# Kernel optimization log

Hardware: AMD Instinct MI355X
Metric: run time of the kernel (lower is better)

The kernel has to match this reference:

```python
import jax, jax.numpy as jnp
import numpy as np

EPS = 1e-12  # F.normalize eps


def setup_inputs() -> dict:
    key = jax.random.key(0)
    k1, k2 = jax.random.split(key)
    bs, d = 8192, 128
    data = jax.random.normal(k1, (bs, d), dtype=jnp.float32)
    label = jax.random.randint(k2, (bs, 1), 0, 2, dtype=jnp.int64)
    scale = jnp.asarray(np.log(1.0 / 0.07), dtype=jnp.float32)  # learned temperature param
    return {"data": data, "scale": scale, "label": label}


def reference(data, scale, label):
    bs = data.shape[0]
    # L2-normalize rows (F.normalize semantics with eps clamp)
    norm = jnp.maximum(jnp.linalg.norm(data, axis=-1, keepdims=True), EPS)
    x = data / norm
    logits = (x @ x.T) * jnp.exp(scale)  # [bs, bs]
    # Vectorized equivalent of the python double loop: binary same-class matrix
    sim = (label == label.T).astype(logits.dtype)  # [bs, bs]
    q = jax.nn.softmax(sim / jnp.sum(sim, axis=-1, keepdims=True), axis=-1)
    p = jax.nn.log_softmax(logits, axis=-1)
    log_q = jnp.log(q)  # q > 0 always (softmax output)
    # F.kl_div(p, q, 'batchmean') = sum(q * (log q - p)) / bs
    loss1 = jnp.sum(q * (log_q - p)) / bs
    # F.kl_div(q.log(), p.exp(), 'batchmean') = sum(exp(p) * (p - log q)) / bs
    loss2 = jnp.sum(jnp.exp(p) * (p - log_q)) / bs
    return (loss1 + loss2) * 0.5
```

## Files before the change

kernel.cpp:

```cpp
#include <hip/hip_runtime.h>
#include <stdint.h>

#define BS 8192
#define DD 128
#define L2E 1.4426950408889634f
#define LN2 0.6931471805599453f

typedef __attribute__((ext_vector_type(8))) short short8;
typedef __attribute__((ext_vector_type(4))) float float4v;

#if __has_builtin(__builtin_amdgcn_exp2f)
#define EXP2(x) __builtin_amdgcn_exp2f(x)
#else
#define EXP2(x) exp2f(x)
#endif

__device__ __forceinline__ float bf2f(short s) {
  union { unsigned u; float f; } c;
  c.u = ((unsigned)(unsigned short)s) << 16;
  return c.f;
}
__device__ __forceinline__ short f2bf(float f) {
  union { float f; unsigned u; } c; c.f = f;
  unsigned u = c.u + 0x7FFFu + ((c.u >> 16) & 1u);
  return (short)(u >> 16);
}


__global__ __launch_bounds__(256) void k_norm(const float* __restrict__ data,
                                              const int* __restrict__ label,
                                              char* __restrict__ xnbF,
                                              float* __restrict__ gh8,
                                              int* __restrict__ cnt8,
                                              float* __restrict__ Zr,
                                              float* __restrict__ Ur,
                                              float* __restrict__ Vr,
                                              float* __restrict__ mf) {
  __shared__ float shg[256];
  __shared__ int shc[2];
  int tid = threadIdx.x, wave = tid >> 6, lane = tid & 63;
  int lh = lane & 31, rsel = lane >> 5;
  if (tid < 2) shc[tid] = 0;
  shg[tid] = 0.f;
  int rowbase = blockIdx.x * 32;
  if (tid < 32) {
    int row = rowbase + tid;
    Zr[row] = 0.f; Ur[row] = 0.f; Vr[row] = 0.f;
    mf[row] = (label[row] == 0) ? 1.f : 0.f;
  }
  __syncthreads();

  float a00 = 0.f, a01 = 0.f, a02 = 0.f, a03 = 0.f;
  float a10 = 0.f, a11 = 0.f, a12 = 0.f, a13 = 0.f;
  int c0 = 0, c1 = 0;
#pragma unroll
  for (int it = 0; it < 4; ++it) {
    int row = rowbase + it * 8 + wave * 2 + rsel;
    float4 v = *(const float4*)&data[row * DD + lh * 4];
    float ss = v.x * v.x + v.y * v.y + v.z * v.z + v.w * v.w;
#pragma unroll
    for (int off = 16; off; off >>= 1) ss += __shfl_xor(ss, off);
    float rn = 1.f / fmaxf(sqrtf(ss), 1e-12f);
    float x0 = v.x * rn, x1 = v.y * rn, x2 = v.z * rn, x3 = v.w * rn;

    unsigned pk0 = (unsigned)(unsigned short)f2bf(x0) |
                   ((unsigned)(unsigned short)f2bf(x1) << 16);
    unsigned pk1 = (unsigned)(unsigned short)f2bf(x2) |
                   ((unsigned)(unsigned short)f2bf(x3) << 16);
    int kc = lh >> 1;
    size_t chunk = (size_t)(row >> 4) * 256 + (size_t)(kc >> 2) * 64 +
                   (size_t)(kc & 3) * 16 + (row & 15);
    *(uint2*)(xnbF + chunk * 16 + (lh & 1) * 8) = make_uint2(pk0, pk1);

    int lab = label[row];
    if (lab == 0) {
      a00 += x0; a01 += x1; a02 += x2; a03 += x3;
      if (lh == 0) c0++;
    } else {
      a10 += x0; a11 += x1; a12 += x2; a13 += x3;
      if (lh == 0) c1++;
    }
  }
  int base = lh * 4;
  atomicAdd(&shg[base + 0], a00); atomicAdd(&shg[base + 1], a01);
  atomicAdd(&shg[base + 2], a02); atomicAdd(&shg[base + 3], a03);
  atomicAdd(&shg[128 + base + 0], a10); atomicAdd(&shg[128 + base + 1], a11);
  atomicAdd(&shg[128 + base + 2], a12); atomicAdd(&shg[128 + base + 3], a13);
  if (lh == 0) { atomicAdd(&shc[0], c0); atomicAdd(&shc[1], c1); }
  __syncthreads();
  atomicAdd(&gh8[(blockIdx.x & 7) * 256 + tid], shg[tid]);
  if (tid < 2) atomicAdd(&cnt8[(blockIdx.x & 7) * 2 + tid], shc[tid]);
}

__global__ __launch_bounds__(512, 4) void k_main(const short* __restrict__ xnbF,
                                                 const int* __restrict__ label,
                                                 const float* __restrict__ mf,
                                                 const float* __restrict__ scale,
                                                 float* __restrict__ Zr,
                                                 float* __restrict__ Ur,
                                                 float* __restrict__ Vr) {
  __shared__ short tile[2][64 * DD];
  int tid = threadIdx.x, wave = tid >> 6, lane = tid & 63;
  int quad = lane >> 4, col = lane & 15;
  int rbI = blockIdx.x >> 4;
  int sl = blockIdx.x & 15;
  float se2 = __expf(scale[0]) * L2E;

  const short8* F = (const short8*)xnbF;

  int gA = rbI * 16 + wave * 2;
  short8 af[2][4];
#pragma unroll
  for (int s = 0; s < 2; ++s)
#pragma unroll
    for (int t = 0; t < 4; ++t) {
      short8 a = F[(size_t)(gA + s) * 256 + t * 64 + lane];
#pragma unroll
      for (int i = 0; i < 8; ++i) a[i] = f2bf(bf2f(a[i]) * se2);
      af[s][t] = a;
    }

  float4v Z0 = {0.f,0.f,0.f,0.f}, Z1 = Z0, U0 = Z0, U1 = Z0, V0 = Z0, V1 = Z0;

  int cb4 = sl * 32;

#define STAGE(buf, jt)                                                         \
  {                                                                            \
    const char* s_ = (const char*)xnbF +                                       \
                     ((size_t)(cb4 + (jt) * 4) * 256 + tid) * 16;              \
    char* d_ = (char*)tile[buf] + tid * 16;                                    \
    __builtin_amdgcn_global_load_lds(                                          \
        (const __attribute__((address_space(1))) void*)(uintptr_t)s_,          \
        (__attribute__((address_space(3))) void*)(uintptr_t)d_, 16, 0, 0);     \
    __builtin_amdgcn_global_load_lds(                                          \
        (const __attribute__((address_space(1))) void*)(uintptr_t)(s_ + 8192), \
        (__attribute__((address_space(3))) void*)(uintptr_t)(d_ + 8192),       \
        16, 0, 0);                                                             \
  }

  STAGE(0, 0);
  __syncthreads();

#pragma unroll 1
  for (int jt = 0; jt < 8; ++jt) {
    if (jt < 7) STAGE((jt + 1) & 1, jt + 1);
    const short8* T8 = (const short8*)tile[jt & 1];
    int jcb = sl * 512 + jt * 64;

#define HALFTILE(jo)                                                           \
    {                                                                          \
      short8 b00 = T8[(jo) * 256 + lane];                                      \
      short8 b01 = T8[(jo) * 256 + 64 + lane];                                 \
      short8 b02 = T8[(jo) * 256 + 128 + lane];                                \
      short8 b03 = T8[(jo) * 256 + 192 + lane];                                \
      short8 b10 = T8[(jo + 1) * 256 + lane];                                  \
      short8 b11 = T8[(jo + 1) * 256 + 64 + lane];                             \
      short8 b12 = T8[(jo + 1) * 256 + 128 + lane];                            \
      short8 b13 = T8[(jo + 1) * 256 + 192 + lane];                            \
      float m0 = mf[jcb + (jo) * 16 + col];                                    \
      float m1 = mf[jcb + (jo + 1) * 16 + col];                                \
      float4v c00 = {0.f, 0.f, 0.f, 0.f}, c01 = c00, c10 = c00, c11 = c00;     \
      c00 = __builtin_amdgcn_mfma_f32_16x16x32_bf16(af[0][0], b00, c00, 0,0,0);\
      c01 = __builtin_amdgcn_mfma_f32_16x16x32_bf16(af[1][0], b00, c01, 0,0,0);\
      c10 = __builtin_amdgcn_mfma_f32_16x16x32_bf16(af[0][0], b10, c10, 0,0,0);\
      c11 = __builtin_amdgcn_mfma_f32_16x16x32_bf16(af[1][0], b10, c11, 0,0,0);\
      c00 = __builtin_amdgcn_mfma_f32_16x16x32_bf16(af[0][1], b01, c00, 0,0,0);\
      c01 = __builtin_amdgcn_mfma_f32_16x16x32_bf16(af[1][1], b01, c01, 0,0,0);\
      c10 = __builtin_amdgcn_mfma_f32_16x16x32_bf16(af[0][1], b11, c10, 0,0,0);\
      c11 = __builtin_amdgcn_mfma_f32_16x16x32_bf16(af[1][1], b11, c11, 0,0,0);\
      c00 = __builtin_amdgcn_mfma_f32_16x16x32_bf16(af[0][2], b02, c00, 0,0,0);\
      c01 = __builtin_amdgcn_mfma_f32_16x16x32_bf16(af[1][2], b02, c01, 0,0,0);\
      c10 = __builtin_amdgcn_mfma_f32_16x16x32_bf16(af[0][2], b12, c10, 0,0,0);\
      c11 = __builtin_amdgcn_mfma_f32_16x16x32_bf16(af[1][2], b12, c11, 0,0,0);\
      c00 = __builtin_amdgcn_mfma_f32_16x16x32_bf16(af[0][3], b03, c00, 0,0,0);\
      c01 = __builtin_amdgcn_mfma_f32_16x16x32_bf16(af[1][3], b03, c01, 0,0,0);\
      c10 = __builtin_amdgcn_mfma_f32_16x16x32_bf16(af[0][3], b13, c10, 0,0,0);\
      c11 = __builtin_amdgcn_mfma_f32_16x16x32_bf16(af[1][3], b13, c11, 0,0,0);\
      _Pragma("unroll")                                                        \
      for (int r = 0; r < 4; ++r) {  \
        float l, e;                                                            \
        l = c00[r]; e = EXP2(l);        \
        Z0[r] += e; U0[r] = fmaf(e, l, U0[r]); V0[r] = fmaf(m0, e, V0[r]);     \
        l = c01[r]; e = EXP2(l);                                               \
        Z1[r] += e; U1[r] = fmaf(e, l, U1[r]); V1[r] = fmaf(m0, e, V1[r]);     \
        l = c10[r]; e = EXP2(l);                                               \
        Z0[r] += e; U0[r] = fmaf(e, l, U0[r]); V0[r] = fmaf(m1, e, V0[r]);     \
        l = c11[r]; e = EXP2(l);                                               \
        Z1[r] += e; U1[r] = fmaf(e, l, U1[r]); V1[r] = fmaf(m1, e, V1[r]);     \
      }                                                                        \
    }
    HALFTILE(0)
    HALFTILE(2)
#undef HALFTILE
    __syncthreads();
  }
#undef STAGE

#define EMIT(s, Zc, Uc, Vc)                                                    \
  {                                                                            \
    _Pragma("unroll")                                                          \
    for (int r = 0; r < 4; ++r) {                                              \
      float z = Zc[r], u = Uc[r], v0 = Vc[r];                                  \
      _Pragma("unroll")                                                        \
      for (int off = 1; off < 16; off <<= 1) {                                 \
        z += __shfl_xor(z, off);                                               \
        u += __shfl_xor(u, off);                                               \
        v0 += __shfl_xor(v0, off);                                             \
      }                                                                        \
      if (col == 0) {                                                          \
        int row = rbI * 256 + wave * 32 + s * 16 + quad * 4 + r;               \
        int lab = label[row];                                                  \
        float v = (lab == 0) ? v0 : (z - v0);                                  \
        atomicAdd(&Zr[row], z);                                                \
        atomicAdd(&Ur[row], u * LN2);                 \
        atomicAdd(&Vr[row], v);                                                \
      }                                                                        \
    }                                                                          \
  }
  EMIT(0, Z0, U0, V0)
  EMIT(1, Z1, U1, V1)
#undef EMIT
}

__global__ __launch_bounds__(256) void k_final(const float* __restrict__ data,
                                               const int* __restrict__ label,
                                               const float* __restrict__ scale,
                                               const float* __restrict__ gh8,
                                               const int* __restrict__ cnt8,
                                               const float* __restrict__ Zr,
                                               const float* __restrict__ Ur,
                                               const float* __restrict__ Vr,
                                               float* __restrict__ partial,
                                               int* __restrict__ ticket,
                                               float* __restrict__ out) {
  __shared__ float hsum[256];
  __shared__ float bsum[4];
  __shared__ int lastb;
  int tid = threadIdx.x, wave = tid >> 6, lane = tid & 63;
  int lh = lane & 31, rsel = lane >> 5;
  float hs = 0.f;
#pragma unroll
  for (int i = 0; i < 8; ++i) hs += gh8[i * 256 + tid];
  hsum[tid] = hs;
  __syncthreads();

  float se = __expf(scale[0]);
  int ci0 = 0, ci1 = 0;
#pragma unroll
  for (int i = 0; i < 8; ++i) { ci0 += cnt8[2 * i]; ci1 += cnt8[2 * i + 1]; }
  float c0 = (float)ci0, c1 = (float)ci1;
  float4 h0 = *(const float4*)&hsum[lh * 4];
  float4 h1 = *(const float4*)&hsum[128 + lh * 4];

  float local = 0.f;
#pragma unroll
  for (int it = 0; it < 4; ++it) {
    int row = blockIdx.x * 32 + it * 8 + wave * 2 + rsel;
    float4 v = *(const float4*)&data[row * DD + lh * 4];
    float ss = v.x * v.x + v.y * v.y + v.z * v.z + v.w * v.w;
#pragma unroll
    for (int off = 16; off; off >>= 1) ss += __shfl_xor(ss, off);
    float rn = 1.f / fmaxf(sqrtf(ss), 1e-12f);

    int lab = label[row];
    float sg = v.x * (h0.x + h1.x) + v.y * (h0.y + h1.y) +
               v.z * (h0.z + h1.z) + v.w * (h0.w + h1.w);
    float sh_ = (lab == 0)
                    ? (v.x * h0.x + v.y * h0.y + v.z * h0.z + v.w * h0.w)
                    : (v.x * h1.x + v.y * h1.y + v.z * h1.z + v.w * h1.w);
#pragma unroll
    for (int off = 16; off; off >>= 1) {
      sg += __shfl_xor(sg, off);
      sh_ += __shfl_xor(sh_, off);
    }
    if (lh == 0) {
      float cc = (lab == 0) ? c0 : c1;
      float a = __expf(1.f / cc);
      float Zq = cc * a + ((float)BS - cc);
      float S = se * sg * rn, T = se * sh_ * rn;
      float Zv = Zr[row], Uv = Ur[row], Vv = Vr[row];
      local += a / Zq - (S + (a - 1.f) * T) / Zq + Uv / Zv - Vv / (cc * Zv);
    }
  }
#pragma unroll
  for (int off = 32; off; off >>= 1) local += __shfl_xor(local, off);
  if (lane == 0) bsum[wave] = local;
  __syncthreads();
  if (tid == 0) {
    float psum = bsum[0] + bsum[1] + bsum[2] + bsum[3];
    __hip_atomic_store(&partial[blockIdx.x], psum, __ATOMIC_RELEASE,
                       __HIP_MEMORY_SCOPE_AGENT);
    int t = __hip_atomic_fetch_add(ticket, 1, __ATOMIC_ACQ_REL,
                                   __HIP_MEMORY_SCOPE_AGENT);
    lastb = (t == 255);
  }
  __syncthreads();
  if (lastb) {
    float v = __hip_atomic_load(&partial[tid], __ATOMIC_ACQUIRE,
                                __HIP_MEMORY_SCOPE_AGENT);
#pragma unroll
    for (int off = 32; off; off >>= 1) v += __shfl_xor(v, off);
    if (lane == 0) bsum[wave] = v;
    __syncthreads();
    if (tid == 0)
      out[0] = (bsum[0] + bsum[1] + bsum[2] + bsum[3]) * (0.5f / (float)BS);
  }
}

extern "C" void kernel_launch(void* const* d_in, const int* in_sizes, int n_in,
                              void* d_out, int out_size, void* d_ws, size_t ws_size,
                              hipStream_t stream) {
  const float* data = (const float*)d_in[0];
  const float* scale = (const float*)d_in[1];
  const int* label = (const int*)d_in[2];
  char* ws = (char*)d_ws;
  char* xnbF = ws;
  float* Zr = (float*)(ws + 2097152);
  float* Ur = (float*)(ws + 2129920);
  float* Vr = (float*)(ws + 2162688);
  float* gh8 = (float*)(ws + 2195456);
  int* cnt8 = (int*)(ws + 2203648);
  int* ticket = (int*)(ws + 2203712);
  float* partial = (float*)(ws + 2203716);
  float* mf = (float*)(ws + 2204800);

  hipMemsetAsync(ws + 2195456, 0, 8260, stream);

  k_norm<<<256, 256, 0, stream>>>(data, label, xnbF, gh8, cnt8, Zr, Ur, Vr, mf);
  k_main<<<512, 512, 0, stream>>>((const short*)xnbF, label, mf, scale, Zr, Ur, Vr);
  k_final<<<256, 256, 0, stream>>>(data, label, scale, gh8, cnt8, Zr, Ur, Vr,
                                   partial, ticket, (float*)d_out);
}
```

Baseline: 108.7 us.

## Exploit Gram matrix symmetry by computing only upper-triangle block pairs

The main kernel now iterates over upper-triangular block pairs (bi<=bj) of the symmetric logits matrix. Off-diagonal tiles feed both row sums and, through per-column reductions and atomics, column sums, which roughly halves the MFMA and exp work. In exchange it adds cross-lane shuffles and many global atomics per tile, and uses a serial loop to decode the triangular index. The norm and final kernels get twice as many smaller blocks and 16-way partial accumulators to match.

After: 162.3 us. +49.3%, slower.

```diff
diff --git a/kernel.cpp b/kernel.cpp
--- a/kernel.cpp
+++ b/kernel.cpp
@@ -30,8 +30,8 @@
 __global__ __launch_bounds__(256) void k_norm(const float* __restrict__ data,
                                               const int* __restrict__ label,
                                               char* __restrict__ xnbF,
-                                              float* __restrict__ gh8,
-                                              int* __restrict__ cnt8,
+                                              float* __restrict__ gh16,
+                                              int* __restrict__ cnt16,
                                               float* __restrict__ Zr,
                                               float* __restrict__ Ur,
                                               float* __restrict__ Vr,
@@ -42,8 +42,8 @@
   int lh = lane & 31, rsel = lane >> 5;
   if (tid < 2) shc[tid] = 0;
   shg[tid] = 0.f;
-  int rowbase = blockIdx.x * 32;
-  if (tid < 32) {
+  int rowbase = blockIdx.x * 16;
+  if (tid < 16) {
     int row = rowbase + tid;
     Zr[row] = 0.f; Ur[row] = 0.f; Vr[row] = 0.f;
     mf[row] = (label[row] == 0) ? 1.f : 0.f;
@@ -54,7 +54,7 @@
   float a10 = 0.f, a11 = 0.f, a12 = 0.f, a13 = 0.f;
   int c0 = 0, c1 = 0;
 #pragma unroll
-  for (int it = 0; it < 4; ++it) {
+  for (int it = 0; it < 2; ++it) {
     int row = rowbase + it * 8 + wave * 2 + rsel;
     float4 v = *(const float4*)&data[row * DD + lh * 4];
     float ss = v.x * v.x + v.y * v.y + v.z * v.z + v.w * v.w;
@@ -88,8 +88,8 @@
   atomicAdd(&shg[128 + base + 2], a12); atomicAdd(&shg[128 + base + 3], a13);
   if (lh == 0) { atomicAdd(&shc[0], c0); atomicAdd(&shc[1], c1); }
   __syncthreads();
-  atomicAdd(&gh8[(blockIdx.x & 7) * 256 + tid], shg[tid]);
-  if (tid < 2) atomicAdd(&cnt8[(blockIdx.x & 7) * 2 + tid], shc[tid]);
+  atomicAdd(&gh16[(blockIdx.x & 15) * 256 + tid], shg[tid]);
+  if (tid < 2) atomicAdd(&cnt16[(blockIdx.x & 15) * 2 + tid], shc[tid]);
 }
 
 __global__ __launch_bounds__(512, 4) void k_main(const short* __restrict__ xnbF,
@@ -102,32 +102,45 @@
   __shared__ short tile[2][64 * DD];
   int tid = threadIdx.x, wave = tid >> 6, lane = tid & 63;
   int quad = lane >> 4, col = lane & 15;
-  int rbI = blockIdx.x >> 4;
-  int sl = blockIdx.x & 15;
+  int job = blockIdx.x;
+  int t = job >> 1, half = job & 1;
+  int bi = 0, rem = t;
+  while (rem >= 32 - bi) { rem -= 32 - bi; ++bi; }
+  int bj = bi + rem;
+  bool offd = (bi != bj);
   float se2 = __expf(scale[0]) * L2E;
 
   const short8* F = (const short8*)xnbF;
 
-  int gA = rbI * 16 + wave * 2;
+  int gA = bi * 16 + wave * 2;
   short8 af[2][4];
 #pragma unroll
   for (int s = 0; s < 2; ++s)
 #pragma unroll
-    for (int t = 0; t < 4; ++t) {
-      short8 a = F[(size_t)(gA + s) * 256 + t * 64 + lane];
+    for (int tt = 0; tt < 4; ++tt) {
+      short8 a = F[(size_t)(gA + s) * 256 + tt * 64 + lane];
 #pragma unroll
       for (int i = 0; i < 8; ++i) a[i] = f2bf(bf2f(a[i]) * se2);
-      af[s][t] = a;
-    }
+      af[s][tt] = a;
+    }
+
+  int rowb = bi * 256 + wave * 32;
+  float mr0[4], mr1[4];
+#pragma unroll
+  for (int r = 0; r < 4; ++r) {
+    mr0[r] = mf[rowb + quad * 4 + r];
+    mr1[r] = mf[rowb + 16 + quad * 4 + r];
+  }
 
   float4v Z0 = {0.f,0.f,0.f,0.f}, Z1 = Z0, U0 = Z0, U1 = Z0, V0 = Z0, V1 = Z0;
 
-  int cb4 = sl * 32;
-
-#define STAGE(buf, jt)                                                         \
+  int cgb = bj * 16 + half * 8;
+  int jbase = bj * 256 + half * 128;
+
+#define STAGE(buf, st)                                                         \
   {                                                                            \
     const char* s_ = (const char*)xnbF +                                       \
-                     ((size_t)(cb4 + (jt) * 4) * 256 + tid) * 16;              \
+                     ((size_t)(cgb + (st) * 4) * 256 + tid) * 16;              \
     char* d_ = (char*)tile[buf] + tid * 16;                                    \
     __builtin_amdgcn_global_load_lds(                                          \
         (const __attribute__((address_space(1))) void*)(uintptr_t)s_,          \
@@ -142,56 +155,50 @@
   __syncthreads();
 
 #pragma unroll 1
-  for (int jt = 0; jt < 8; ++jt) {
-    if (jt < 7) STAGE((jt + 1) & 1, jt + 1);
-    const short8* T8 = (const short8*)tile[jt & 1];
-    int jcb = sl * 512 + jt * 64;
-
-#define HALFTILE(jo)                                                           \
-    {                                                                          \
-      short8 b00 = T8[(jo) * 256 + lane];                                      \
-      short8 b01 = T8[(jo) * 256 + 64 + lane];                                 \
-      short8 b02 = T8[(jo) * 256 + 128 + lane];                                \
-      short8 b03 = T8[(jo) * 256 + 192 + lane];                                \
-      short8 b10 = T8[(jo + 1) * 256 + lane];                                  \
-      short8 b11 = T8[(jo + 1) * 256 + 64 + lane];                             \
-      short8 b12 = T8[(jo + 1) * 256 + 128 + lane];                            \
-      short8 b13 = T8[(jo + 1) * 256 + 192 + lane];                            \
-      float m0 = mf[jcb + (jo) * 16 + col];                                    \
-      float m1 = mf[jcb + (jo + 1) * 16 + col];                                \
-      float4v c00 = {0.f, 0.f, 0.f, 0.f}, c01 = c00, c10 = c00, c11 = c00;     \
-      c00 = __builtin_amdgcn_mfma_f32_16x16x32_bf16(af[0][0], b00, c00, 0,0,0);\
-      c01 = __builtin_amdgcn_mfma_f32_16x16x32_bf16(af[1][0], b00, c01, 0,0,0);\
-      c10 = __builtin_amdgcn_mfma_f32_16x16x32_bf16(af[0][0], b10, c10, 0,0,0);\
-      c11 = __builtin_amdgcn_mfma_f32_16x16x32_bf16(af[1][0], b10, c11, 0,0,0);\
-      c00 = __builtin_amdgcn_mfma_f32_16x16x32_bf16(af[0][1], b01, c00, 0,0,0);\
-      c01 = __builtin_amdgcn_mfma_f32_16x16x32_bf16(af[1][1], b01, c01, 0,0,0);\
-      c10 = __builtin_amdgcn_mfma_f32_16x16x32_bf16(af[0][1], b11, c10, 0,0,0);\
-      c11 = __builtin_amdgcn_mfma_f32_16x16x32_bf16(af[1][1], b11, c11, 0,0,0);\
-      c00 = __builtin_amdgcn_mfma_f32_16x16x32_bf16(af[0][2], b02, c00, 0,0,0);\
-      c01 = __builtin_amdgcn_mfma_f32_16x16x32_bf16(af[1][2], b02, c01, 0,0,0);\
-      c10 = __builtin_amdgcn_mfma_f32_16x16x32_bf16(af[0][2], b12, c10, 0,0,0);\
-      c11 = __builtin_amdgcn_mfma_f32_16x16x32_bf16(af[1][2], b12, c11, 0,0,0);\
-      c00 = __builtin_amdgcn_mfma_f32_16x16x32_bf16(af[0][3], b03, c00, 0,0,0);\
-      c01 = __builtin_amdgcn_mfma_f32_16x16x32_bf16(af[1][3], b03, c01, 0,0,0);\
-      c10 = __builtin_amdgcn_mfma_f32_16x16x32_bf16(af[0][3], b13, c10, 0,0,0);\
-      c11 = __builtin_amdgcn_mfma_f32_16x16x32_bf16(af[1][3], b13, c11, 0,0,0);\
-      _Pragma("unroll")                                                        \
-      for (int r = 0; r < 4; ++r) {  \
-        float l, e;                                                            \
-        l = c00[r]; e = EXP2(l);        \
-        Z0[r] += e; U0[r] = fmaf(e, l, U0[r]); V0[r] = fmaf(m0, e, V0[r]);     \
-        l = c01[r]; e = EXP2(l);                                               \
-        Z1[r] += e; U1[r] = fmaf(e, l, U1[r]); V1[r] = fmaf(m0, e, V1[r]);     \
-        l = c10[r]; e = EXP2(l);                                               \
-        Z0[r] += e; U0[r] = fmaf(e, l, U0[r]); V0[r] = fmaf(m1, e, V0[r]);     \
-        l = c11[r]; e = EXP2(l);                                               \
-        Z1[r] += e; U1[r] = fmaf(e, l, U1[r]); V1[r] = fmaf(m1, e, V1[r]);     \
-      }                                                                        \
-    }
-    HALFTILE(0)
-    HALFTILE(2)
-#undef HALFTILE
+  for (int st = 0; st < 2; ++st) {
+    if (st == 0) STAGE(1, 1);
+    const short8* T8 = (const short8*)tile[st];
+    int jcb = jbase + st * 64;
+#pragma unroll
+    for (int jo = 0; jo < 4; ++jo) {
+      short8 b0 = T8[jo * 256 + lane];
+      short8 b1 = T8[jo * 256 + 64 + lane];
+      short8 b2 = T8[jo * 256 + 128 + lane];
+      short8 b3 = T8[jo * 256 + 192 + lane];
+      float m0 = mf[jcb + jo * 16 + col];
+      float4v c0 = {0.f, 0.f, 0.f, 0.f}, c1 = c0;
+      c0 = __builtin_amdgcn_mfma_f32_16x16x32_bf16(af[0][0], b0, c0, 0, 0, 0);
+      c1 = __builtin_amdgcn_mfma_f32_16x16x32_bf16(af[1][0], b0, c1, 0, 0, 0);
+      c0 = __builtin_amdgcn_mfma_f32_16x16x32_bf16(af[0][1], b1, c0, 0, 0, 0);
+      c1 = __builtin_amdgcn_mfma_f32_16x16x32_bf16(af[1][1], b1, c1, 0, 0, 0);
+      c0 = __builtin_amdgcn_mfma_f32_16x16x32_bf16(af[0][2], b2, c0, 0, 0, 0);
+      c1 = __builtin_amdgcn_mfma_f32_16x16x32_bf16(af[1][2], b2, c1, 0, 0, 0);
+      c0 = __builtin_amdgcn_mfma_f32_16x16x32_bf16(af[0][3], b3, c0, 0, 0, 0);
+      c1 = __builtin_amdgcn_mfma_f32_16x16x32_bf16(af[1][3], b3, c1, 0, 0, 0);
+      float zc = 0.f, uc = 0.f, vc = 0.f;
+#pragma unroll
+      for (int r = 0; r < 4; ++r) {
+        float l = c0[r], e = EXP2(l);
+        Z0[r] += e; U0[r] = fmaf(e, l, U0[r]); V0[r] = fmaf(m0, e, V0[r]);
+        zc += e; uc = fmaf(e, l, uc); vc = fmaf(mr0[r], e, vc);
+        l = c1[r]; e = EXP2(l);
+        Z1[r] += e; U1[r] = fmaf(e, l, U1[r]); V1[r] = fmaf(m0, e, V1[r]);
+        zc += e; uc = fmaf(e, l, uc); vc = fmaf(mr1[r], e, vc);
+      }
+      if (offd) {
+        zc += __shfl_xor(zc, 16); uc += __shfl_xor(uc, 16);
+        vc += __shfl_xor(vc, 16);
+        zc += __shfl_xor(zc, 32); uc += __shfl_xor(uc, 32);
+        vc += __shfl_xor(vc, 32);
+        if (quad == 0) {
+          int jc = jcb + jo * 16 + col;
+          atomicAdd(&Zr[jc], zc);
+          atomicAdd(&Ur[jc], uc * LN2);
+          float vcol = (m0 != 0.f) ? vc : (zc - vc);
+          atomicAdd(&Vr[jc], vcol);
+        }
+      }
+    }
     __syncthreads();
   }
 #undef STAGE
@@ -208,7 +215,7 @@
         v0 += __shfl_xor(v0, off);                                             \
       }                                                                        \
       if (col == 0) {                                                          \
-        int row = rbI * 256 + wave * 32 + s * 16 + quad * 4 + r;               \
+        int row = rowb + s * 16 + quad * 4 + r;                                \
         int lab = label[row];                                                  \
         float v = (lab == 0) ? v0 : (z - v0);                                  \
         atomicAdd(&Zr[row], z);                                                \
@@ -225,8 +232,8 @@
 __global__ __launch_bounds__(256) void k_final(const float* __restrict__ data,
                                                const int* __restrict__ label,
                                                const float* __restrict__ scale,
-                                               const float* __restrict__ gh8,
-                                               const int* __restrict__ cnt8,
+                                               const float* __restrict__ gh16,
+                                               const int* __restrict__ cnt16,
                                                const float* __restrict__ Zr,
                                                const float* __restrict__ Ur,
                                                const float* __restrict__ Vr,
@@ -240,22 +247,22 @@
   int lh = lane & 31, rsel = lane >> 5;
   float hs = 0.f;
 #pragma unroll
-  for (int i = 0; i < 8; ++i) hs += gh8[i * 256 + tid];
+  for (int i = 0; i < 16; ++i) hs += gh16[i * 256 + tid];
   hsum[tid] = hs;
   __syncthreads();
 
   float se = __expf(scale[0]);
   int ci0 = 0, ci1 = 0;
 #pragma unroll
-  for (int i = 0; i < 8; ++i) { ci0 += cnt8[2 * i]; ci1 += cnt8[2 * i + 1]; }
+  for (int i = 0; i < 16; ++i) { ci0 += cnt16[2 * i]; ci1 += cnt16[2 * i + 1]; }
   float c0 = (float)ci0, c1 = (float)ci1;
   float4 h0 = *(const float4*)&hsum[lh * 4];
   float4 h1 = *(const float4*)&hsum[128 + lh * 4];
 
   float local = 0.f;
 #pragma unroll
-  for (int it = 0; it < 4; ++it) {
-    int row = blockIdx.x * 32 + it * 8 + wave * 2 + rsel;
+  for (int it = 0; it < 2; ++it) {
+    int row = blockIdx.x * 16 + it * 8 + wave * 2 + rsel;
     float4 v = *(const float4*)&data[row * DD + lh * 4];
     float ss = v.x * v.x + v.y * v.y + v.z * v.z + v.w * v.w;
 #pragma unroll
@@ -292,11 +299,13 @@
                        __HIP_MEMORY_SCOPE_AGENT);
     int t = __hip_atomic_fetch_add(ticket, 1, __ATOMIC_ACQ_REL,
                                    __HIP_MEMORY_SCOPE_AGENT);
-    lastb = (t == 255);
+    lastb = (t == 511);
   }
   __syncthreads();
   if (lastb) {
     float v = __hip_atomic_load(&partial[tid], __ATOMIC_ACQUIRE,
+                                __HIP_MEMORY_SCOPE_AGENT) +
+              __hip_atomic_load(&partial[tid + 256], __ATOMIC_ACQUIRE,
                                 __HIP_MEMORY_SCOPE_AGENT);
 #pragma unroll
     for (int off = 32; off; off >>= 1) v += __shfl_xor(v, off);
@@ -318,16 +327,16 @@
   float* Zr = (float*)(ws + 2097152);
   float* Ur = (float*)(ws + 2129920);
   float* Vr = (float*)(ws + 2162688);
-  float* gh8 = (float*)(ws + 2195456);
-  int* cnt8 = (int*)(ws + 2203648);
-  int* ticket = (int*)(ws + 2203712);
-  float* partial = (float*)(ws + 2203716);
-  float* mf = (float*)(ws + 2204800);
-
-  hipMemsetAsync(ws + 2195456, 0, 8260, stream);
-
-  k_norm<<<256, 256, 0, stream>>>(data, label, xnbF, gh8, cnt8, Zr, Ur, Vr, mf);
-  k_main<<<512, 512, 0, stream>>>((const short*)xnbF, label, mf, scale, Zr, Ur, Vr);
-  k_final<<<256, 256, 0, stream>>>(data, label, scale, gh8, cnt8, Zr, Ur, Vr,
+  float* gh16 = (float*)(ws + 2195456);
+  int* cnt16 = (int*)(ws + 2211840);
+  int* ticket = (int*)(ws + 2211968);
+  float* partial = (float*)(ws + 2211972);
+  float* mf = (float*)(ws + 2214020);
+
+  hipMemsetAsync(ws + 2195456, 0, 16516, stream);
+
+  k_norm<<<512, 256, 0, stream>>>(data, label, xnbF, gh16, cnt16, Zr, Ur, Vr, mf);
+  k_main<<<1056, 512, 0, stream>>>((const short*)xnbF, label, mf, scale, Zr, Ur, Vr);
+  k_final<<<512, 256, 0, stream>>>(data, label, scale, gh16, cnt16, Zr, Ur, Vr,
                                    partial, ticket, (float*)d_out);
 }
```

## Fold final reduction into main kernel and accumulate logit sums in-loop

Applied to the files above, without the earlier changes.

Removes the k_final kernel and the per-class feature-sum histogram in k_norm. The main GEMM loop now also accumulates the raw logit sum and the same-class logit sum per row, which replaces the separate data re-read and dot-product pass. The last-arriving block of k_main, detected with a ticket counter, computes the final loss. This saves one kernel launch and the extra pass over the data, at the cost of extra ALU work and two more atomics per row inside the hot loop, plus a serial tail reduction on a single block. k_norm is also relaunched with more, smaller blocks.

Measured after the change: 117.1 us. 7.7% more time.

```diff
diff --git a/kernel.cpp b/kernel.cpp
--- a/kernel.cpp
+++ b/kernel.cpp
@@ -30,31 +30,22 @@
 __global__ __launch_bounds__(256) void k_norm(const float* __restrict__ data,
                                               const int* __restrict__ label,
                                               char* __restrict__ xnbF,
-                                              float* __restrict__ gh8,
-                                              int* __restrict__ cnt8,
                                               float* __restrict__ Zr,
                                               float* __restrict__ Ur,
                                               float* __restrict__ Vr,
+                                              float* __restrict__ Wr,
+                                              float* __restrict__ Xr,
                                               float* __restrict__ mf) {
-  __shared__ float shg[256];
-  __shared__ int shc[2];
   int tid = threadIdx.x, wave = tid >> 6, lane = tid & 63;
   int lh = lane & 31, rsel = lane >> 5;
-  if (tid < 2) shc[tid] = 0;
-  shg[tid] = 0.f;
-  int rowbase = blockIdx.x * 32;
-  if (tid < 32) {
+  int rowbase = blockIdx.x * 16;
+  if (tid < 16) {
     int row = rowbase + tid;
-    Zr[row] = 0.f; Ur[row] = 0.f; Vr[row] = 0.f;
+    Zr[row] = 0.f; Ur[row] = 0.f; Vr[row] = 0.f; Wr[row] = 0.f; Xr[row] = 0.f;
     mf[row] = (label[row] == 0) ? 1.f : 0.f;
   }
-  __syncthreads();
-
-  float a00 = 0.f, a01 = 0.f, a02 = 0.f, a03 = 0.f;
-  float a10 = 0.f, a11 = 0.f, a12 = 0.f, a13 = 0.f;
-  int c0 = 0, c1 = 0;
-#pragma unroll
-  for (int it = 0; it < 4; ++it) {
+#pragma unroll
+  for (int it = 0; it < 2; ++it) {
     int row = rowbase + it * 8 + wave * 2 + rsel;
     float4 v = *(const float4*)&data[row * DD + lh * 4];
     float ss = v.x * v.x + v.y * v.y + v.z * v.z + v.w * v.w;
@@ -71,25 +62,7 @@
     size_t chunk = (size_t)(row >> 4) * 256 + (size_t)(kc >> 2) * 64 +
                    (size_t)(kc & 3) * 16 + (row & 15);
     *(uint2*)(xnbF + chunk * 16 + (lh & 1) * 8) = make_uint2(pk0, pk1);
-
-    int lab = label[row];
-    if (lab == 0) {
-      a00 += x0; a01 += x1; a02 += x2; a03 += x3;
-      if (lh == 0) c0++;
-    } else {
-      a10 += x0; a11 += x1; a12 += x2; a13 += x3;
-      if (lh == 0) c1++;
-    }
-  }
-  int base = lh * 4;
-  atomicAdd(&shg[base + 0], a00); atomicAdd(&shg[base + 1], a01);
-  atomicAdd(&shg[base + 2], a02); atomicAdd(&shg[base + 3], a03);
-  atomicAdd(&shg[128 + base + 0], a10); atomicAdd(&shg[128 + base + 1], a11);
-  atomicAdd(&shg[128 + base + 2], a12); atomicAdd(&shg[128 + base + 3], a13);
-  if (lh == 0) { atomicAdd(&shc[0], c0); atomicAdd(&shc[1], c1); }
-  __syncthreads();
-  atomicAdd(&gh8[(blockIdx.x & 7) * 256 + tid], shg[tid]);
-  if (tid < 2) atomicAdd(&cnt8[(blockIdx.x & 7) * 2 + tid], shc[tid]);
+  }
 }
 
 __global__ __launch_bounds__(512, 4) void k_main(const short* __restrict__ xnbF,
@@ -98,8 +71,15 @@
                                                  const float* __restrict__ scale,
                                                  float* __restrict__ Zr,
                                                  float* __restrict__ Ur,
-                                                 float* __restrict__ Vr) {
+                                                 float* __restrict__ Vr,
+                                                 float* __restrict__ Wr,
+                                                 float* __restrict__ Xr,
+                                                 int* __restrict__ ticket,
+                                                 float* __restrict__ out) {
   __shared__ short tile[2][64 * DD];
+  __shared__ int credu[8];
+  __shared__ float fredu[8];
+  __shared__ int lastf;
   int tid = threadIdx.x, wave = tid >> 6, lane = tid & 63;
   int quad = lane >> 4, col = lane & 15;
   int rbI = blockIdx.x >> 4;
@@ -107,7 +87,6 @@
   float se2 = __expf(scale[0]) * L2E;
 
   const short8* F = (const short8*)xnbF;
-
   int gA = rbI * 16 + wave * 2;
   short8 af[2][4];
 #pragma unroll
@@ -121,7 +100,7 @@
     }
 
   float4v Z0 = {0.f,0.f,0.f,0.f}, Z1 = Z0, U0 = Z0, U1 = Z0, V0 = Z0, V1 = Z0;
-
+  float4v W0 = Z0, W1 = Z0, X0 = Z0, X1 = Z0;
   int cb4 = sl * 32;
 
 #define STAGE(buf, jt)                                                         \
@@ -181,12 +160,16 @@
         float l, e;                                                            \
         l = c00[r]; e = EXP2(l);        \
         Z0[r] += e; U0[r] = fmaf(e, l, U0[r]); V0[r] = fmaf(m0, e, V0[r]);     \
+        W0[r] += l; X0[r] = fmaf(m0, l, X0[r]);                                \
         l = c01[r]; e = EXP2(l);                                               \
         Z1[r] += e; U1[r] = fmaf(e, l, U1[r]); V1[r] = fmaf(m0, e, V1[r]);     \
+        W1[r] += l; X1[r] = fmaf(m0, l, X1[r]);                                \
         l = c10[r]; e = EXP2(l);                                               \
         Z0[r] += e; U0[r] = fmaf(e, l, U0[r]); V0[r] = fmaf(m1, e, V0[r]);     \
+        W0[r] += l; X0[r] = fmaf(m1, l, X0[r]);                                \
         l = c11[r]; e = EXP2(l);                                               \
         Z1[r] += e; U1[r] = fmaf(e, l, U1[r]); V1[r] = fmaf(m1, e, V1[r]);     \
+        W1[r] += l; X1[r] = fmaf(m1, l, X1[r]);                                \
       }                                                                        \
     }
     HALFTILE(0)
@@ -196,114 +179,89 @@
   }
 #undef STAGE
 
-#define EMIT(s, Zc, Uc, Vc)                                                    \
+#define EMIT(s, Zc, Uc, Vc, Wc, Xc)                                            \
   {                                                                            \
     _Pragma("unroll")                                                          \
     for (int r = 0; r < 4; ++r) {                                              \
-      float z = Zc[r], u = Uc[r], v0 = Vc[r];                                  \
+      float z = Zc[r], u = Uc[r], v0 = Vc[r], w = Wc[r], x0 = Xc[r];           \
       _Pragma("unroll")                                                        \
       for (int off = 1; off < 16; off <<= 1) {                                 \
         z += __shfl_xor(z, off);                                               \
         u += __shfl_xor(u, off);                                               \
         v0 += __shfl_xor(v0, off);                                             \
+        w += __shfl_xor(w, off);                                               \
+        x0 += __shfl_xor(x0, off);                                             \
       }                                                                        \
       if (col == 0) {                                                          \
         int row = rbI * 256 + wave * 32 + s * 16 + quad * 4 + r;               \
         int lab = label[row];                                                  \
         float v = (lab == 0) ? v0 : (z - v0);                                  \
+        float x = (lab == 0) ? x0 : (w - x0);                                  \
         atomicAdd(&Zr[row], z);                                                \
         atomicAdd(&Ur[row], u * LN2);                 \
         atomicAdd(&Vr[row], v);                                                \
+        atomicAdd(&Wr[row], w * LN2);        \
+        atomicAdd(&Xr[row], x * LN2);                         \
       }                                                                        \
     }                                                                          \
   }
-  EMIT(0, Z0, U0, V0)
-  EMIT(1, Z1, U1, V1)
+  EMIT(0, Z0, U0, V0, W0, X0)
+  EMIT(1, Z1, U1, V1, W1, X1)
 #undef EMIT
-}
-
-__global__ __launch_bounds__(256) void k_final(const float* __restrict__ data,
-                                               const int* __restrict__ label,
-                                               const float* __restrict__ scale,
-                                               const float* __restrict__ gh8,
-                                               const int* __restrict__ cnt8,
-                                               const float* __restrict__ Zr,
-                                               const float* __restrict__ Ur,
-                                               const float* __restrict__ Vr,
-                                               float* __restrict__ partial,
-                                               int* __restrict__ ticket,
-                                               float* __restrict__ out) {
-  __shared__ float hsum[256];
-  __shared__ float bsum[4];
-  __shared__ int lastb;
-  int tid = threadIdx.x, wave = tid >> 6, lane = tid & 63;
-  int lh = lane & 31, rsel = lane >> 5;
-  float hs = 0.f;
-#pragma unroll
-  for (int i = 0; i < 8; ++i) hs += gh8[i * 256 + tid];
-  hsum[tid] = hs;
-  __syncthreads();
-
-  float se = __expf(scale[0]);
-  int ci0 = 0, ci1 = 0;
-#pragma unroll
-  for (int i = 0; i < 8; ++i) { ci0 += cnt8[2 * i]; ci1 += cnt8[2 * i + 1]; }
-  float c0 = (float)ci0, c1 = (float)ci1;
-  float4 h0 = *(const float4*)&hsum[lh * 4];
-  float4 h1 = *(const float4*)&hsum[128 + lh * 4];
-
-  float local = 0.f;
-#pragma unroll
-  for (int it = 0; it < 4; ++it) {
-    int row = blockIdx.x * 32 + it * 8 + wave * 2 + rsel;
-    float4 v = *(const float4*)&data[row * DD + lh * 4];
-    float ss = v.x * v.x + v.y * v.y + v.z * v.z + v.w * v.w;
-#pragma unroll
-    for (int off = 16; off; off >>= 1) ss += __shfl_xor(ss, off);
-    float rn = 1.f / fmaxf(sqrtf(ss), 1e-12f);
-
-    int lab = label[row];
-    float sg = v.x * (h0.x + h1.x) + v.y * (h0.y + h1.y) +
-               v.z * (h0.z + h1.z) + v.w * (h0.w + h1.w);
-    float sh_ = (lab == 0)
-                    ? (v.x * h0.x + v.y * h0.y + v.z * h0.z + v.w * h0.w)
-                    : (v.x * h1.x + v.y * h1.y + v.z * h1.z + v.w * h1.w);
-#pragma unroll
-    for (int off = 16; off; off >>= 1) {
-      sg += __shfl_xor(sg, off);
-      sh_ += __shfl_xor(sh_, off);
-    }
-    if (lh == 0) {
-      float cc = (lab == 0) ? c0 : c1;
-      float a = __expf(1.f / cc);
-      float Zq = cc * a + ((float)BS - cc);
-      float S = se * sg * rn, T = se * sh_ * rn;
-      float Zv = Zr[row], Uv = Ur[row], Vv = Vr[row];
-      local += a / Zq - (S + (a - 1.f) * T) / Zq + Uv / Zv - Vv / (cc * Zv);
-    }
-  }
-#pragma unroll
-  for (int off = 32; off; off >>= 1) local += __shfl_xor(local, off);
-  if (lane == 0) bsum[wave] = local;
+
   __syncthreads();
   if (tid == 0) {
-    float psum = bsum[0] + bsum[1] + bsum[2] + bsum[3];
-    __hip_atomic_store(&partial[blockIdx.x], psum, __ATOMIC_RELEASE,
-                       __HIP_MEMORY_SCOPE_AGENT);
     int t = __hip_atomic_fetch_add(ticket, 1, __ATOMIC_ACQ_REL,
                                    __HIP_MEMORY_SCOPE_AGENT);
-    lastb = (t == 255);
-  }
-  __syncthreads();
-  if (lastb) {
-    float v = __hip_atomic_load(&partial[tid], __ATOMIC_ACQUIRE,
-                                __HIP_MEMORY_SCOPE_AGENT);
-#pragma unroll
-    for (int off = 32; off; off >>= 1) v += __shfl_xor(v, off);
-    if (lane == 0) bsum[wave] = v;
-    __syncthreads();
-    if (tid == 0)
-      out[0] = (bsum[0] + bsum[1] + bsum[2] + bsum[3]) * (0.5f / (float)BS);
+    lastf = (t == 511);
+  }
+  __syncthreads();
+  if (!lastf) return;
+
+  int labs[16];
+  int c1i = 0;
+#pragma unroll
+  for (int k = 0; k < 16; ++k) {
+    labs[k] = label[k * 512 + tid];
+    c1i += labs[k];
+  }
+#pragma unroll
+  for (int off = 32; off; off >>= 1) c1i += __shfl_xor(c1i, off);
+  if (lane == 0) credu[wave] = c1i;
+  __syncthreads();
+  int c1t = 0;
+#pragma unroll
+  for (int w = 0; w < 8; ++w) c1t += credu[w];
+  float c1 = (float)c1t, c0 = (float)(BS - c1t);
+  float a0 = __expf(1.f / c0), a1 = __expf(1.f / c1);
+  float rZq0 = 1.f / (c0 * a0 + ((float)BS - c0));
+  float rZq1 = 1.f / (c1 * a1 + ((float)BS - c1));
+  float rc0 = 1.f / c0, rc1 = 1.f / c1;
+
+  float local = 0.f;
+#pragma unroll
+  for (int k = 0; k < 16; ++k) {
+    int row = k * 512 + tid;
+    float Z = __hip_atomic_load(&Zr[row], __ATOMIC_RELAXED, __HIP_MEMORY_SCOPE_AGENT);
+    float U = __hip_atomic_load(&Ur[row], __ATOMIC_RELAXED, __HIP_MEMORY_SCOPE_AGENT);
+    float V = __hip_atomic_load(&Vr[row], __ATOMIC_RELAXED, __HIP_MEMORY_SCOPE_AGENT);
+    float S = __hip_atomic_load(&Wr[row], __ATOMIC_RELAXED, __HIP_MEMORY_SCOPE_AGENT);
+    float T = __hip_atomic_load(&Xr[row], __ATOMIC_RELAXED, __HIP_MEMORY_SCOPE_AGENT);
+    int lab = labs[k];
+    float a = lab ? a1 : a0;
+    float rZq = lab ? rZq1 : rZq0;
+    float rc = lab ? rc1 : rc0;
+    local += rZq * (a - S - (a - 1.f) * T) + (U - V * rc) / Z;
+  }
+#pragma unroll
+  for (int off = 32; off; off >>= 1) local += __shfl_xor(local, off);
+  if (lane == 0) fredu[wave] = local;
+  __syncthreads();
+  if (tid == 0) {
+    float s = 0.f;
+#pragma unroll
+    for (int w = 0; w < 8; ++w) s += fredu[w];
+    out[0] = s * (0.5f / (float)BS);
   }
 }
 
@@ -318,16 +276,14 @@
   float* Zr = (float*)(ws + 2097152);
   float* Ur = (float*)(ws + 2129920);
   float* Vr = (float*)(ws + 2162688);
-  float* gh8 = (float*)(ws + 2195456);
-  int* cnt8 = (int*)(ws + 2203648);
-  int* ticket = (int*)(ws + 2203712);
-  float* partial = (float*)(ws + 2203716);
-  float* mf = (float*)(ws + 2204800);
-
-  hipMemsetAsync(ws + 2195456, 0, 8260, stream);
-
-  k_norm<<<256, 256, 0, stream>>>(data, label, xnbF, gh8, cnt8, Zr, Ur, Vr, mf);
-  k_main<<<512, 512, 0, stream>>>((const short*)xnbF, label, mf, scale, Zr, Ur, Vr);
-  k_final<<<256, 256, 0, stream>>>(data, label, scale, gh8, cnt8, Zr, Ur, Vr,
-                                   partial, ticket, (float*)d_out);
-}
+  float* Wr = (float*)(ws + 2195456);
+  float* Xr = (float*)(ws + 2228224);
+  float* mf = (float*)(ws + 2260992);
+  int* ticket = (int*)(ws + 2293760);
+
+  hipMemsetAsync(ws + 2293760, 0, 4, stream);
+
+  k_norm<<<512, 256, 0, stream>>>(data, label, xnbF, Zr, Ur, Vr, Wr, Xr, mf);
+  k_main<<<512, 512, 0, stream>>>((const short*)xnbF, label, mf, scale, Zr, Ur,
+                                  Vr, Wr, Xr, ticket, (float*)d_out);
+}
```
